# Performance work log

Measured on AMD Instinct MI355X. Metric: run time of the kernel, lower is better.

The kernel has to match this reference:

```python
import jax, jax.numpy as jnp
import numpy as np

N, E, H, L = 20000, 1_280_000, 64, 4


def setup_inputs() -> dict:
    key = jax.random.key(0)
    ks = jax.random.split(key, 24)
    inputs = jax.random.normal(ks[0], (1, N, 6), jnp.float32)
    node_masks = jnp.ones((1, N), jnp.int32)
    send_edges = jax.random.randint(ks[1], (E,), 0, N)
    recv_edges = jax.random.randint(ks[2], (E,), 0, N)

    def w(k, shape, scale=None):
        s = (1.0 / np.sqrt(shape[-2])) if scale is None else scale
        return (jax.random.normal(k, shape, jnp.float32) * s)

    d = dict(
        inputs=inputs, node_masks=node_masks,
        send_edges=send_edges, recv_edges=recv_edges,
        emb_w=w(ks[3], (1, H)), emb_b=jnp.zeros((H,), jnp.float32),
        edge_w1=w(ks[4], (L, 2 * H + 1, H)), edge_b1=jnp.zeros((L, H), jnp.float32),
        edge_w2=w(ks[5], (L, H, H)), edge_b2=jnp.zeros((L, H), jnp.float32),
        node_w1=w(ks[6], (L, 2 * H, H)), node_b1=jnp.zeros((L, H), jnp.float32),
        node_w2=w(ks[7], (L, H, H)), node_b2=jnp.zeros((L, H), jnp.float32),
        coord_w1=w(ks[8], (L, H, H)), coord_b1=jnp.zeros((L, H), jnp.float32),
        coord_wout=w(ks[9], (L, H, 1), scale=0.001),  # xavier gain=0.001, no bias
        vel_w1=w(ks[10], (L, H, H)), vel_b1=jnp.zeros((L, H), jnp.float32),
        vel_w2=w(ks[11], (L, H, 1)), vel_b2=jnp.zeros((L, 1), jnp.float32),
    )
    return d


def reference(inputs, node_masks, send_edges, recv_edges,
              emb_w, emb_b, edge_w1, edge_b1, edge_w2, edge_b2,
              node_w1, node_b1, node_w2, node_b2,
              coord_w1, coord_b1, coord_wout,
              vel_w1, vel_b1, vel_w2, vel_b2):
    silu = jax.nn.silu
    # node_masks is all-ones -> node_inds = arange(N); all nodes active.
    pos, vel = jnp.split(inputs, 2, axis=-1)          # [1,N,3] each
    h = jnp.linalg.norm(vel, axis=-1, keepdims=True)  # speed -> [1,N,1]
    h = h @ emb_w + emb_b                             # [1,N,H]
    coord = pos
    n = coord.shape[1]
    counts = jax.ops.segment_sum(jnp.ones_like(recv_edges, dtype=coord.dtype),
                                 recv_edges, num_segments=n)
    inv_cnt = (1.0 / jnp.maximum(counts, 1.0))[None, :, None]
    seg = lambda e: jax.ops.segment_sum(e, recv_edges, num_segments=n)

    for l in range(L):
        # coord2radial
        cd = coord[:, send_edges] - coord[:, recv_edges]        # [1,E,3]
        radial = jnp.sum(cd * cd, -1, keepdims=True)            # [1,E,1]
        # edge_model
        ef_in = jnp.concatenate([h[:, send_edges], h[:, recv_edges], radial], -1)
        ef = silu(silu(ef_in @ edge_w1[l] + edge_b1[l]) @ edge_w2[l] + edge_b2[l])
        # coord_model
        cm = silu(ef @ coord_w1[l] + coord_b1[l]) @ coord_wout[l]  # [1,E,1]
        trans = jnp.clip(cd * cm, -100.0, 100.0)
        agg_mean = jax.vmap(seg)(trans) * inv_cnt                  # scatter_mean
        # velocity update
        v_gate = silu(h @ vel_w1[l] + vel_b1[l]) @ vel_w2[l] + vel_b2[l]
        vel = agg_mean + v_gate * vel
        coord = coord + vel
        # node_model (recurrent residual)
        agg_sum = jax.vmap(seg)(ef)                                # scatter_sum
        hn = jnp.concatenate([h, agg_sum], -1)
        h = silu(hn @ node_w1[l] + node_b1[l]) @ node_w2[l] + node_b2[l] + h

    pred = jnp.concatenate([coord, vel], -1)  # [1,N,6] == pred_all (all active)
    return pred
```

## Files before the change

kernel.cpp:

```cpp
#include <hip/hip_runtime.h>
#include <math.h>

#define N_NODES 20000
#define N_EDGES 1280000
#define NLAYERS 4
#define NTILE (N_EDGES/32)
#define TSTRIDE 68

typedef short bf16x8 __attribute__((ext_vector_type(8)));
typedef float f32x4  __attribute__((ext_vector_type(4)));
typedef long long i64;
typedef unsigned short us;

__device__ __forceinline__ float silu_f(float x) {
    return x / (1.0f + __expf(-x));
}

__device__ __forceinline__ us f2b(float x) {
    union { float f; unsigned u; } v; v.f = x;
    unsigned r = v.u + 0x7FFF + ((v.u >> 16) & 1);
    return (us)(r >> 16);
}
__device__ __forceinline__ float b2f(us u) {
    union { float f; unsigned u; } v; v.u = ((unsigned)u) << 16;
    return v.f;
}
__device__ __forceinline__ void split2r(float x, us& hi, us& lo) {
    hi = f2b(x);
    lo = f2b(x - b2f(hi));
}
__device__ __forceinline__ void split2f(float x, us& hi, us& lo) {
    union { float f; unsigned u; } v; v.f = x;
    hi = (us)(v.u >> 16);
    union { float f; unsigned u; } h; h.u = v.u & 0xFFFF0000u;
    union { float f; unsigned u; } r; r.f = x - h.f;
    lo = (us)(r.u >> 16);
}

__device__ __forceinline__ bf16x8 ld8(const us* p) {
    bf16x8 a;
    ((i64*)&a)[0] = *(const i64*)p;
    ((i64*)&a)[1] = *(const i64*)(p + 4);
    return a;
}

__device__ __forceinline__ void mfma3(f32x4& acc, bf16x8 ahi, bf16x8 alo,
                                      bf16x8 bhi, bf16x8 blo) {
    acc = __builtin_amdgcn_mfma_f32_16x16x32_bf16(ahi, bhi, acc, 0, 0, 0);
    acc = __builtin_amdgcn_mfma_f32_16x16x32_bf16(alo, bhi, acc, 0, 0, 0);
    acc = __builtin_amdgcn_mfma_f32_16x16x32_bf16(ahi, blo, acc, 0, 0, 0);
}

__global__ void k_init(const float* __restrict__ inp,
                       const float* __restrict__ emb_w,
                       const float* __restrict__ emb_b,
                       float* __restrict__ outv,
                       us* __restrict__ hbh, us* __restrict__ hbl) {
    int t = blockIdx.x * blockDim.x + threadIdx.x;
    int n = t >> 6, f = t & 63;
    if (n >= N_NODES) return;
    float vx = inp[n*6+3], vy = inp[n*6+4], vz = inp[n*6+5];
    float sp = sqrtf(vx*vx + vy*vy + vz*vz);
    float hv = sp * emb_w[f] + emb_b[f];
    us hi, lo; split2r(hv, hi, lo);
    hbh[t] = hi; hbl[t] = lo;
    if (f < 6) outv[n*6+f] = inp[n*6+f];
}

__global__ void k_cnt(const int* __restrict__ recv, int* __restrict__ counts) {
    int t = blockIdx.x*256 + threadIdx.x;
    if (t < N_EDGES) atomicAdd(&counts[recv[t]], 1);
}

__global__ void k_scan(const int* __restrict__ counts, int* __restrict__ rowstart,
                       int* __restrict__ cursor) {
    __shared__ int buf[256];
    __shared__ int carry;
    const int tid = threadIdx.x;
    if (tid == 0) carry = 0;
    __syncthreads();
    for (int base = 0; base < N_NODES; base += 256) {
        const int i = base + tid;
        int v = (i < N_NODES) ? counts[i] : 0;
        buf[tid] = v;
        __syncthreads();
        for (int off = 1; off < 256; off <<= 1) {
            int tv = (tid >= off) ? buf[tid-off] : 0;
            __syncthreads();
            buf[tid] += tv;
            __syncthreads();
        }
        const int excl = buf[tid] - v;
        if (i < N_NODES) { int rv = carry + excl; rowstart[i] = rv; cursor[i] = rv; }
        __syncthreads();
        if (tid == 255) carry += buf[255];
        __syncthreads();
    }
    if (tid < 20) rowstart[N_NODES + tid] = N_EDGES;
}

__global__ void k_scatter(const int* __restrict__ send, const int* __restrict__ recv,
                          int* __restrict__ cursor, us* __restrict__ sp16) {
    int t = blockIdx.x*256 + threadIdx.x;
    if (t < N_EDGES) {
        int p = atomicAdd(&cursor[recv[t]], 1);
        sp16[p] = (us)send[t];
    }
}

__global__ void k_tilemap(const int* __restrict__ rowstart, int* __restrict__ tile2node) {
    int b = blockIdx.x*256 + threadIdx.x;
    if (b >= NTILE) return;
    const int e = b*32;
    int lo = 0, hi = N_NODES-1;
    while (lo < hi) {
        int mid = (lo+hi+1) >> 1;
        if (rowstart[mid] <= e) lo = mid; else hi = mid-1;
    }
    tile2node[b] = lo;
}

__global__ void k_prepw(const float* __restrict__ ew1, const float* __restrict__ ew2,
                        const float* __restrict__ cw1,
                        us* __restrict__ w1th, us* __restrict__ w1tl,
                        us* __restrict__ w2th, us* __restrict__ w2tl,
                        us* __restrict__ cw1th, us* __restrict__ cw1tl) {
    int t = blockIdx.x*256 + threadIdx.x;
    int l = t >> 14;
    int r = t & 16383;
    us hi, lo;
    if (r < 8192) {
        int n = r >> 7, k = r & 127;
        split2r(ew1[l*129*64 + k*64 + n], hi, lo);
        w1th[l*8192 + r] = hi; w1tl[l*8192 + r] = lo;
    } else if (r < 12288) {
        int rr = r - 8192; int n = rr >> 6, k = rr & 63;
        split2r(ew2[l*4096 + k*64 + n], hi, lo);
        w2th[l*4096 + n*64 + k] = hi; w2tl[l*4096 + n*64 + k] = lo;
    } else {
        int rr = r - 12288; int n = rr >> 6, k = rr & 63;
        split2r(cw1[l*4096 + k*64 + n], hi, lo);
        cw1th[l*4096 + n*64 + k] = hi; cw1tl[l*4096 + n*64 + k] = lo;
    }
}

__launch_bounds__(256, 4)
__global__ void k_edge(const us* __restrict__ sp16, const int* __restrict__ rowstart,
                       const int* __restrict__ tile2node,
                       const us* __restrict__ hbh, const us* __restrict__ hbl,
                       const float* __restrict__ outv,
                       const us* __restrict__ w1th, const us* __restrict__ w1tl,
                       const us* __restrict__ w2th, const us* __restrict__ w2tl,
                       const us* __restrict__ cw1th, const us* __restrict__ cw1tl,
                       const float* __restrict__ ew1, const float* __restrict__ eb1,
                       const float* __restrict__ eb2, const float* __restrict__ cb1,
                       const float* __restrict__ cwo,
                       float* __restrict__ aggs, float* __restrict__ aggm) {
    __shared__ us tileh[4][32*TSTRIDE];
    __shared__ us tilel[4][32*TSTRIDE];

    const int tid  = threadIdx.x;
    const int wid  = tid >> 6;
    const int lane = tid & 63;
    const int q    = lane >> 4;
    const int l15  = lane & 15;
    const int wbase = blockIdx.x*128 + wid*32;
    const int wtile = blockIdx.x*4 + wid;

    const int e0 = wbase + l15, e1 = e0 + 16;
    const int s0 = sp16[e0], s1 = sp16[e1];

    const int t2n = tile2node[wtile];
    const int wv = rowstart[t2n + 1 + l15];
    int seg0 = 0, seg1 = 0;
    #pragma unroll
    for (int i = 0; i < 16; ++i) {
        const int wi = __shfl(wv, i);
        seg0 += (e0 >= wi);
        seg1 += (e1 >= wi);
    }
    const int r0 = t2n + seg0, r1 = t2n + seg1;

    const float cdx0 = outv[s0*6+0]-outv[r0*6+0], cdy0 = outv[s0*6+1]-outv[r0*6+1], cdz0 = outv[s0*6+2]-outv[r0*6+2];
    const float cdx1 = outv[s1*6+0]-outv[r1*6+0], cdy1 = outv[s1*6+1]-outv[r1*6+1], cdz1 = outv[s1*6+2]-outv[r1*6+2];
    const float rad0 = cdx0*cdx0+cdy0*cdy0+cdz0*cdz0;
    const float rad1 = cdx1*cdx1+cdy1*cdy1+cdz1*cdz1;

    f32x4 acc[2][4];
    #pragma unroll
    for (int mu = 0; mu < 2; ++mu)
        #pragma unroll
        for (int t = 0; t < 4; ++t) acc[mu][t] = (f32x4){0.f,0.f,0.f,0.f};

    #pragma unroll
    for (int kc = 0; kc < 4; ++kc) {
        const int off = (kc & 1)*32 + q*8;
        const size_t o0 = (size_t)((kc < 2) ? s0 : r0)*64 + off;
        const size_t o1 = (size_t)((kc < 2) ? s1 : r1)*64 + off;
        bf16x8 a0h = ld8(hbh + o0), a0l = ld8(hbl + o0);
        bf16x8 a1h = ld8(hbh + o1), a1l = ld8(hbl + o1);
        #pragma unroll
        for (int t = 0; t < 4; ++t) {
            const int wo = (16*t + l15)*128 + kc*32 + q*8;
            bf16x8 bh = ld8(w1th + wo), bl = ld8(w1tl + wo);
            mfma3(acc[0][t], a0h, a0l, bh, bl);
            mfma3(acc[1][t], a1h, a1l, bh, bl);
        }
    }

    float rsh0[4], rsh1[4];
    #pragma unroll
    for (int r = 0; r < 4; ++r) {
        rsh0[r] = __shfl(rad0, 4*q + r);
        rsh1[r] = __shfl(rad1, 4*q + r);
    }
    #pragma unroll
    for (int t = 0; t < 4; ++t) {
        const int col = 16*t + l15;
        const float wl = ew1[128*64 + col];
        const float bb = eb1[col];
        #pragma unroll
        for (int r = 0; r < 4; ++r) {
            acc[0][t][r] += rsh0[r]*wl + bb;
            acc[1][t][r] += rsh1[r]*wl + bb;
        }
    }

    us* Th = tileh[wid];
    us* Tl = tilel[wid];
    #pragma unroll
    for (int mu = 0; mu < 2; ++mu)
        #pragma unroll
        for (int t = 0; t < 4; ++t)
            #pragma unroll
            for (int r = 0; r < 4; ++r) {
                us hi, lo; split2f(silu_f(acc[mu][t][r]), hi, lo);
                const int ti = (mu*16 + 4*q + r)*TSTRIDE + 16*t + l15;
                Th[ti] = hi; Tl[ti] = lo;
            }
    __asm__ volatile("s_waitcnt lgkmcnt(0)" ::: "memory");

    #pragma unroll
    for (int mu = 0; mu < 2; ++mu)
        #pragma unroll
        for (int t = 0; t < 4; ++t) acc[mu][t] = (f32x4){0.f,0.f,0.f,0.f};
    #pragma unroll
    for (int kc = 0; kc < 2; ++kc) {
        const int t0 = l15*TSTRIDE + kc*32 + q*8;
        const int t1i = (16+l15)*TSTRIDE + kc*32 + q*8;
        bf16x8 a0h = ld8(Th + t0),  a0l = ld8(Tl + t0);
        bf16x8 a1h = ld8(Th + t1i), a1l = ld8(Tl + t1i);
        #pragma unroll
        for (int t = 0; t < 4; ++t) {
            const int wo = (16*t + l15)*64 + kc*32 + q*8;
            bf16x8 bh = ld8(w2th + wo), bl = ld8(w2tl + wo);
            mfma3(acc[0][t], a0h, a0l, bh, bl);
            mfma3(acc[1][t], a1h, a1l, bh, bl);
        }
    }

    float ef[2][4][4];
    #pragma unroll
    for (int t = 0; t < 4; ++t) {
        const float bb = eb2[16*t + l15];
        #pragma unroll
        for (int mu = 0; mu < 2; ++mu)
            #pragma unroll
            for (int r = 0; r < 4; ++r)
                ef[mu][t][r] = silu_f(acc[mu][t][r] + bb);
    }
    __asm__ volatile("s_waitcnt lgkmcnt(0)" ::: "memory");
    #pragma unroll
    for (int mu = 0; mu < 2; ++mu)
        #pragma unroll
        for (int t = 0; t < 4; ++t)
            #pragma unroll
            for (int r = 0; r < 4; ++r) {
                us hi, lo; split2f(ef[mu][t][r], hi, lo);
                const int ti = (mu*16 + 4*q + r)*TSTRIDE + 16*t + l15;
                Th[ti] = hi; Tl[ti] = lo;
            }
    __asm__ volatile("s_waitcnt lgkmcnt(0)" ::: "memory");

    #pragma unroll
    for (int mu = 0; mu < 2; ++mu)
        #pragma unroll
        for (int t = 0; t < 4; ++t) acc[mu][t] = (f32x4){0.f,0.f,0.f,0.f};
    #pragma unroll
    for (int kc = 0; kc < 2; ++kc) {
        const int t0 = l15*TSTRIDE + kc*32 + q*8;
        const int t1i = (16+l15)*TSTRIDE + kc*32 + q*8;
        bf16x8 a0h = ld8(Th + t0),  a0l = ld8(Tl + t0);
        bf16x8 a1h = ld8(Th + t1i), a1l = ld8(Tl + t1i);
        #pragma unroll
        for (int t = 0; t < 4; ++t) {
            const int wo = (16*t + l15)*64 + kc*32 + q*8;
            bf16x8 bh = ld8(cw1th + wo), bl = ld8(cw1tl + wo);
            mfma3(acc[0][t], a0h, a0l, bh, bl);
            mfma3(acc[1][t], a1h, a1l, bh, bl);
        }
    }

    float cm0[4] = {0.f,0.f,0.f,0.f}, cm1[4] = {0.f,0.f,0.f,0.f};
    #pragma unroll
    for (int t = 0; t < 4; ++t) {
        const int col = 16*t + l15;
        const float cb = cb1[col];
        const float co = cwo[col];
        #pragma unroll
        for (int r = 0; r < 4; ++r) {
            cm0[r] += silu_f(acc[0][t][r] + cb) * co;
            cm1[r] += silu_f(acc[1][t][r] + cb) * co;
        }
    }
    #pragma unroll
    for (int m = 1; m <= 8; m <<= 1)
        #pragma unroll
        for (int r = 0; r < 4; ++r) {
            cm0[r] += __shfl_xor(cm0[r], m);
            cm1[r] += __shfl_xor(cm1[r], m);
        }

    int   sgrow[2][4];
    float tv[2][4];
    #pragma unroll
    for (int mu = 0; mu < 2; ++mu)
        #pragma unroll
        for (int r = 0; r < 4; ++r) {
            sgrow[mu][r] = __shfl(mu ? seg1 : seg0, 4*q + r);
            const float cxv = __shfl(mu ? cdx1 : cdx0, 4*q + r);
            const float cyv = __shfl(mu ? cdy1 : cdy0, 4*q + r);
            const float czv = __shfl(mu ? cdz1 : cdz0, 4*q + r);
            const float cmv = mu ? cm1[r] : cm0[r];
            const float sel = (l15 == 0) ? cxv : (l15 == 1) ? cyv : czv;
            tv[mu][r] = (l15 < 3) ? fminf(fmaxf(sel*cmv, -100.f), 100.f) : 0.f;
        }

    const int segA = __shfl(seg0, 0);
    const int segB = __shfl(seg1, 15);

    if (segB == segA) {
        float s4[4], trT = 0.f;
        #pragma unroll
        for (int t = 0; t < 4; ++t) {
            float v = 0.f;
            #pragma unroll
            for (int mu = 0; mu < 2; ++mu)
                #pragma unroll
                for (int r = 0; r < 4; ++r) v += ef[mu][t][r];
            v += __shfl_xor(v, 16);
            v += __shfl_xor(v, 32);
            s4[t] = v;
        }
        #pragma unroll
        for (int mu = 0; mu < 2; ++mu)
            #pragma unroll
            for (int r = 0; r < 4; ++r) trT += tv[mu][r];
        trT += __shfl_xor(trT, 16);
        trT += __shfl_xor(trT, 32);
        const int rn = t2n + segA;
        if (q == 0) {
            #pragma unroll
            for (int t = 0; t < 4; ++t)
                atomicAdd(&aggs[(size_t)rn*64 + 16*t + l15], s4[t]);
            if (l15 < 3) atomicAdd(&aggm[rn*3 + l15], trT);
        }
    } else if (segB == segA + 1) {
        float sA[4] = {0,0,0,0}, sB[4] = {0,0,0,0};
        float trA = 0.f, trB = 0.f;
        #pragma unroll
        for (int mu = 0; mu < 2; ++mu)
            #pragma unroll
            for (int r = 0; r < 4; ++r) {
                const bool isA = (sgrow[mu][r] == segA);
                #pragma unroll
                for (int t = 0; t < 4; ++t) {
                    const float v = ef[mu][t][r];
                    sA[t] += isA ? v : 0.f;
                    sB[t] += isA ? 0.f : v;
                }
                const float tvv = tv[mu][r];
                trA += isA ? tvv : 0.f;
                trB += isA ? 0.f : tvv;
            }
        #pragma unroll
        for (int t = 0; t < 4; ++t) {
            sA[t] += __shfl_xor(sA[t], 16); sA[t] += __shfl_xor(sA[t], 32);
            sB[t] += __shfl_xor(sB[t], 16); sB[t] += __shfl_xor(sB[t], 32);
        }
        trA += __shfl_xor(trA, 16); trA += __shfl_xor(trA, 32);
        trB += __shfl_xor(trB, 16); trB += __shfl_xor(trB, 32);
        const int rnA = t2n + segA, rnB = rnA + 1;
        if (q == 0) {
            #pragma unroll
            for (int t = 0; t < 4; ++t) {
                atomicAdd(&aggs[(size_t)rnA*64 + 16*t + l15], sA[t]);
                atomicAdd(&aggs[(size_t)rnB*64 + 16*t + l15], sB[t]);
            }
            if (l15 < 3) {
                atomicAdd(&aggm[rnA*3 + l15], trA);
                atomicAdd(&aggm[rnB*3 + l15], trB);
            }
        }
    } else {
        #pragma unroll
        for (int mu = 0; mu < 2; ++mu)
            #pragma unroll
            for (int r = 0; r < 4; ++r) {
                const int ren = t2n + sgrow[mu][r];
                #pragma unroll
                for (int t = 0; t < 4; ++t)
                    atomicAdd(&aggs[(size_t)ren*64 + 16*t + l15], ef[mu][t][r]);
                if (l15 < 3) atomicAdd(&aggm[ren*3 + l15], tv[mu][r]);
            }
    }
}

__launch_bounds__(256, 4)
__global__ void k_node(const float* __restrict__ aggs, const float* __restrict__ aggm,
                       const int* __restrict__ rowstart,
                       const float* __restrict__ VW1, const float* __restrict__ vb1,
                       const float* __restrict__ VW2, const float* __restrict__ vb2,
                       const float* __restrict__ NW1, const float* __restrict__ nb1,
                       const float* __restrict__ NW2, const float* __restrict__ nb2,
                       float* __restrict__ outv,
                       us* __restrict__ hbh, us* __restrict__ hbl) {
    __shared__ float hs[4][64], as[4][64], tt[4][64];
    const int tid = threadIdx.x;
    const int nn = tid >> 6, f = tid & 63;
    const int n = blockIdx.x*4 + nn;
    float hv = b2f(hbh[n*64+f]) + b2f(hbl[n*64+f]);
    hs[nn][f] = hv;
    as[nn][f] = aggs[n*64+f];
    __syncthreads();

    float a1 = vb1[f];
    for (int k = 0; k < 64; ++k) a1 += hs[nn][k] * VW1[k*64+f];
    float p = silu_f(a1) * VW2[f];
    #pragma unroll
    for (int o = 32; o > 0; o >>= 1) p += __shfl_down(p, o);
    float vgate = __shfl(p, 0) + vb2[0];

    if (f < 3) {
        float icnt = 1.0f / fmaxf((float)(rowstart[n+1] - rowstart[n]), 1.0f);
        float nv = aggm[n*3+f]*icnt + vgate*outv[n*6+3+f];
        outv[n*6+3+f] = nv;
        outv[n*6+f]  += nv;
    }

    float b = nb1[f];
    for (int k = 0; k < 64; ++k) b += hs[nn][k]*NW1[k*64+f];
    for (int k = 0; k < 64; ++k) b += as[nn][k]*NW1[(64+k)*64+f];
    __syncthreads();
    tt[nn][f] = silu_f(b);
    __syncthreads();
    float o = nb2[f] + hv;
    for (int k = 0; k < 64; ++k) o += tt[nn][k]*NW2[k*64+f];
    us hi, lo; split2r(o, hi, lo);
    hbh[n*64+f] = hi; hbl[n*64+f] = lo;
}

extern "C" void kernel_launch(void* const* d_in, const int* in_sizes, int n_in,
                              void* d_out, int out_size, void* d_ws, size_t ws_size,
                              hipStream_t stream) {
    const float* inp   = (const float*)d_in[0];
    const int*   send  = (const int*)d_in[2];
    const int*   recv  = (const int*)d_in[3];
    const float* emb_w = (const float*)d_in[4];
    const float* emb_b = (const float*)d_in[5];
    const float* ew1   = (const float*)d_in[6];
    const float* eb1   = (const float*)d_in[7];
    const float* ew2   = (const float*)d_in[8];
    const float* eb2   = (const float*)d_in[9];
    const float* nw1   = (const float*)d_in[10];
    const float* nb1   = (const float*)d_in[11];
    const float* nw2   = (const float*)d_in[12];
    const float* nb2   = (const float*)d_in[13];
    const float* cw1   = (const float*)d_in[14];
    const float* cb1   = (const float*)d_in[15];
    const float* cwo   = (const float*)d_in[16];
    const float* vw1   = (const float*)d_in[17];
    const float* vb1   = (const float*)d_in[18];
    const float* vw2   = (const float*)d_in[19];
    const float* vb2   = (const float*)d_in[20];

    float* outv = (float*)d_out;

    float* ws        = (float*)d_ws;
    float* aggs      = ws;
    float* aggm      = aggs + (size_t)N_NODES*64;
    int*   rowstart  = (int*)(aggm + N_NODES*3);
    int*   tile2node = rowstart + (N_NODES+20);
    us*    hbh       = (us*)(tile2node + NTILE);
    us*    hbl       = hbh + (size_t)N_NODES*64;
    us*    sp16      = hbl + (size_t)N_NODES*64;
    us*    w1th      = sp16 + N_EDGES;
    us*    w1tl      = w1th + 4*8192;
    us*    w2th      = w1tl + 4*8192;
    us*    w2tl      = w2th + 4*4096;
    us*    cw1th     = w2tl + 4*4096;
    us*    cw1tl     = cw1th + 4*4096;
    int*   counts    = (int*)aggs;
    int*   cursor    = counts + N_NODES;

    hipMemsetAsync(counts, 0, N_NODES*sizeof(int), stream);
    k_init<<<(N_NODES*64)/256, 256, 0, stream>>>(inp, emb_w, emb_b, outv, hbh, hbl);
    k_cnt<<<(N_EDGES+255)/256, 256, 0, stream>>>(recv, counts);
    k_scan<<<1, 256, 0, stream>>>(counts, rowstart, cursor);
    k_scatter<<<(N_EDGES+255)/256, 256, 0, stream>>>(send, recv, cursor, sp16);
    k_tilemap<<<(NTILE+255)/256, 256, 0, stream>>>(rowstart, tile2node);
    k_prepw<<<256, 256, 0, stream>>>(ew1, ew2, cw1, w1th, w1tl, w2th, w2tl, cw1th, cw1tl);

    for (int l = 0; l < NLAYERS; ++l) {
        hipMemsetAsync(aggs, 0, (size_t)N_NODES*67*sizeof(float), stream);
        k_edge<<<N_EDGES/128, 256, 0, stream>>>(sp16, rowstart, tile2node, hbh, hbl, outv,
            w1th + l*8192, w1tl + l*8192,
            w2th + l*4096, w2tl + l*4096,
            cw1th + l*4096, cw1tl + l*4096,
            ew1 + (size_t)l*129*64, eb1 + l*64, eb2 + l*64,
            cb1 + l*64, cwo + l*64,
            aggs, aggm);
        k_node<<<N_NODES/4, 256, 0, stream>>>(aggs, aggm, rowstart,
            vw1 + (size_t)l*64*64, vb1 + l*64, vw2 + l*64, vb2 + l,
            nw1 + (size_t)l*128*64, nb1 + l*64,
            nw2 + (size_t)l*64*64,  nb2 + l*64,
            outv, hbh, hbl);
    }
}
```

Before: 2.082 ms.

## Fold tilemap into scan, clear aggregates in node kernel, halve edge block size

The single-block scan now gives each thread a contiguous chunk of nodes, which replaces many serial 256-wide passes, and it fills tile2node directly, so the separate binary-search k_tilemap kernel is removed. The per-layer memset of the aggregation buffers is replaced by having k_node zero aggs and aggm after reading them, leaving only one memset before the loop. k_edge now runs 128-thread blocks with half the shared-memory tiles, which gives finer-grained scheduling. Together these cut launch and preprocessing overhead, though the chunked scan reads counts serially per thread with strided access.

```diff
diff --git a/kernel.cpp b/kernel.cpp
--- a/kernel.cpp
+++ b/kernel.cpp
@@ -6,6 +6,7 @@
 #define NLAYERS 4
 #define NTILE (N_EDGES/32)
 #define TSTRIDE 68
+#define SCHUNK 79
 
 typedef short bf16x8 __attribute__((ext_vector_type(8)));
 typedef float f32x4  __attribute__((ext_vector_type(4)));
@@ -73,28 +74,27 @@
 }
 
 __global__ void k_scan(const int* __restrict__ counts, int* __restrict__ rowstart,
-                       int* __restrict__ cursor) {
+                       int* __restrict__ cursor, int* __restrict__ tile2node) {
     __shared__ int buf[256];
-    __shared__ int carry;
     const int tid = threadIdx.x;
-    if (tid == 0) carry = 0;
+    const int lo = tid*SCHUNK;
+    const int hi = (lo + SCHUNK < N_NODES) ? lo + SCHUNK : N_NODES;
+    int s = 0;
+    for (int i = lo; i < hi; ++i) s += counts[i];
+    buf[tid] = s;
     __syncthreads();
-    for (int base = 0; base < N_NODES; base += 256) {
-        const int i = base + tid;
-        int v = (i < N_NODES) ? counts[i] : 0;
-        buf[tid] = v;
+    for (int off = 1; off < 256; off <<= 1) {
+        int v = (tid >= off) ? buf[tid-off] : 0;
         __syncthreads();
-        for (int off = 1; off < 256; off <<= 1) {
-            int tv = (tid >= off) ? buf[tid-off] : 0;
-            __syncthreads();
-            buf[tid] += tv;
-            __syncthreads();
-        }
-        const int excl = buf[tid] - v;
-        if (i < N_NODES) { int rv = carry + excl; rowstart[i] = rv; cursor[i] = rv; }
+        buf[tid] += v;
         __syncthreads();
-        if (tid == 255) carry += buf[255];
-        __syncthreads();
+    }
+    int run = buf[tid] - s;
+    for (int i = lo; i < hi; ++i) {
+        rowstart[i] = run; cursor[i] = run;
+        const int c = counts[i];
+        for (int t = (run + 31) >> 5; t*32 < run + c; ++t) tile2node[t] = i;
+        run += c;
     }
     if (tid < 20) rowstart[N_NODES + tid] = N_EDGES;
 }
@@ -106,18 +106,6 @@
         int p = atomicAdd(&cursor[recv[t]], 1);
         sp16[p] = (us)send[t];
     }
-}
-
-__global__ void k_tilemap(const int* __restrict__ rowstart, int* __restrict__ tile2node) {
-    int b = blockIdx.x*256 + threadIdx.x;
-    if (b >= NTILE) return;
-    const int e = b*32;
-    int lo = 0, hi = N_NODES-1;
-    while (lo < hi) {
-        int mid = (lo+hi+1) >> 1;
-        if (rowstart[mid] <= e) lo = mid; else hi = mid-1;
-    }
-    tile2node[b] = lo;
 }
 
 __global__ void k_prepw(const float* __restrict__ ew1, const float* __restrict__ ew2,
@@ -144,7 +132,7 @@
     }
 }
 
-__launch_bounds__(256, 4)
+__launch_bounds__(128, 4)
 __global__ void k_edge(const us* __restrict__ sp16, const int* __restrict__ rowstart,
                        const int* __restrict__ tile2node,
                        const us* __restrict__ hbh, const us* __restrict__ hbl,
@@ -156,16 +144,16 @@
                        const float* __restrict__ eb2, const float* __restrict__ cb1,
                        const float* __restrict__ cwo,
                        float* __restrict__ aggs, float* __restrict__ aggm) {
-    __shared__ us tileh[4][32*TSTRIDE];
-    __shared__ us tilel[4][32*TSTRIDE];
+    __shared__ us tileh[2][32*TSTRIDE];
+    __shared__ us tilel[2][32*TSTRIDE];
 
     const int tid  = threadIdx.x;
     const int wid  = tid >> 6;
     const int lane = tid & 63;
     const int q    = lane >> 4;
     const int l15  = lane & 15;
-    const int wbase = blockIdx.x*128 + wid*32;
-    const int wtile = blockIdx.x*4 + wid;
+    const int wbase = blockIdx.x*64 + wid*32;
+    const int wtile = blockIdx.x*2 + wid;
 
     const int e0 = wbase + l15, e1 = e0 + 16;
     const int s0 = sp16[e0], s1 = sp16[e1];
@@ -417,7 +405,7 @@
 }
 
 __launch_bounds__(256, 4)
-__global__ void k_node(const float* __restrict__ aggs, const float* __restrict__ aggm,
+__global__ void k_node(float* __restrict__ aggs, float* __restrict__ aggm,
                        const int* __restrict__ rowstart,
                        const float* __restrict__ VW1, const float* __restrict__ vb1,
                        const float* __restrict__ VW2, const float* __restrict__ vb2,
@@ -432,6 +420,7 @@
     float hv = b2f(hbh[n*64+f]) + b2f(hbl[n*64+f]);
     hs[nn][f] = hv;
     as[nn][f] = aggs[n*64+f];
+    aggs[n*64+f] = 0.f;
     __syncthreads();
 
     float a1 = vb1[f];
@@ -444,6 +433,7 @@
     if (f < 3) {
         float icnt = 1.0f / fmaxf((float)(rowstart[n+1] - rowstart[n]), 1.0f);
         float nv = aggm[n*3+f]*icnt + vgate*outv[n*6+3+f];
+        aggm[n*3+f] = 0.f;
         outv[n*6+3+f] = nv;
         outv[n*6+f]  += nv;
     }
@@ -506,14 +496,13 @@
     hipMemsetAsync(counts, 0, N_NODES*sizeof(int), stream);
     k_init<<<(N_NODES*64)/256, 256, 0, stream>>>(inp, emb_w, emb_b, outv, hbh, hbl);
     k_cnt<<<(N_EDGES+255)/256, 256, 0, stream>>>(recv, counts);
-    k_scan<<<1, 256, 0, stream>>>(counts, rowstart, cursor);
+    k_scan<<<1, 256, 0, stream>>>(counts, rowstart, cursor, tile2node);
     k_scatter<<<(N_EDGES+255)/256, 256, 0, stream>>>(send, recv, cursor, sp16);
-    k_tilemap<<<(NTILE+255)/256, 256, 0, stream>>>(rowstart, tile2node);
     k_prepw<<<256, 256, 0, stream>>>(ew1, ew2, cw1, w1th, w1tl, w2th, w2tl, cw1th, cw1tl);
+    hipMemsetAsync(aggs, 0, (size_t)N_NODES*67*sizeof(float), stream);
 
     for (int l = 0; l < NLAYERS; ++l) {
-        hipMemsetAsync(aggs, 0, (size_t)N_NODES*67*sizeof(float), stream);
-        k_edge<<<N_EDGES/128, 256, 0, stream>>>(sp16, rowstart, tile2node, hbh, hbl, outv,
+        k_edge<<<N_EDGES/64, 128, 0, stream>>>(sp16, rowstart, tile2node, hbh, hbl, outv,
             w1th + l*8192, w1tl + l*8192,
             w2th + l*4096, w2tl + l*4096,
             cw1th + l*4096, cw1tl + l*4096,
```

After: 2.047 ms. Within noise of the previous version (-1.7%).
